# Kernel tuning notes

Hardware: AMD Instinct MI355X
Metric: run time of the kernel (lower is better)

The kernel has to match this reference:

```python
import jax, jax.numpy as jnp
import numpy as np

N_NODES = 81920
N_EDGES = 1310720
NODES_PER_GRAPH = 320
N_GRAPHS = N_NODES // NODES_PER_GRAPH  # 256
IN_DIM = 64
HID = 64
OUT = 64


def setup_inputs() -> dict:
    key = jax.random.key(0)
    ks = jax.random.split(key, 16)
    x = jax.random.normal(ks[0], (N_NODES, IN_DIM), dtype=jnp.float32)
    edge_index = jax.random.randint(ks[1], (2, N_EDGES), 0, N_NODES, dtype=jnp.int32)
    # sorted graph-membership vector: 256 graphs of 320 nodes each
    batch = (jnp.arange(N_NODES, dtype=jnp.int32) // NODES_PER_GRAPH)
    std = 1.0  # module re-inits nn.Linear weights with N(0, 1)
    dims = [(IN_DIM, HID), (HID, HID), (HID, OUT)]
    params = {}
    for i, (di, do) in enumerate(dims):
        params[f"Wl{i}"] = std * jax.random.normal(ks[2 + 3 * i], (di, do), dtype=jnp.float32)
        params[f"bl{i}"] = jnp.zeros((do,), dtype=jnp.float32)
        params[f"Wr{i}"] = std * jax.random.normal(ks[3 + 3 * i], (di, do), dtype=jnp.float32)
    return dict(x=x, edge_index=edge_index, batch=batch, **params)


def _sage_conv(x, src, dst, Wl, bl, Wr):
    # PyG SAGEConv (aggr='mean', root_weight=True):
    #   out = lin_l(mean_{j in N(i)} x_j) + lin_r(x_i)
    msg = x[src]                                              # [E, d] gather
    agg = jax.ops.segment_sum(msg, dst, num_segments=N_NODES)  # [N, d] scatter-add
    cnt = jax.ops.segment_sum(jnp.ones((src.shape[0],), x.dtype), dst,
                              num_segments=N_NODES)
    agg = agg / jnp.maximum(cnt, 1.0)[:, None]                # mean aggregation
    return agg @ Wl + bl + x @ Wr


def reference(x, edge_index, batch, Wl0, bl0, Wr0, Wl1, bl1, Wr1, Wl2, bl2, Wr2):
    src, dst = edge_index[0], edge_index[1]
    layers = [(Wl0, bl0, Wr0), (Wl1, bl1, Wr1), (Wl2, bl2, Wr2)]
    h = x
    for i, (Wl, bl, Wr) in enumerate(layers):
        h = _sage_conv(h, src, dst, Wl, bl, Wr)
        if i < len(layers) - 1:
            h = jax.nn.relu(h)
            # F.dropout is identity in eval mode (training=False)
    # unbatch + take node 0 of every graph: first index where batch == g
    first_idx = jnp.searchsorted(batch, jnp.arange(N_GRAPHS, dtype=batch.dtype))
    return h[first_idx]  # [N_GRAPHS, OUT]
```

## Files before the change

kernel.cpp:

```cpp
#include <hip/hip_runtime.h>

#define N_NODES 81920
#define N_EDGES 1310720
#define NG 256
#define D 64
#define TM 64
#define SA 65
#define SB 33
#define NB 320
#define NBLK 1280
#define BMW 2560
#define HCHUNK 4096
#define EPT 16
#define CAP0 1280
#define CAP1 256
#define CAP2 64

typedef __attribute__((ext_vector_type(2))) short sbf2;

__device__ __forceinline__ bool tb(const unsigned* bm, int i) {
    return (bm[i >> 5] >> (i & 31)) & 1u;
}
__device__ __forceinline__ unsigned bf16rne(float f) {
    unsigned u = __float_as_uint(f);
    return (u + 0x7fffu + ((u >> 16) & 1u)) >> 16;
}


__global__ __launch_bounds__(256) void init_ws(float4* __restrict__ aggb4,
                                               unsigned* __restrict__ bms,
                                               int* __restrict__ indeg,
                                               int* __restrict__ n01,
                                               int* __restrict__ cur0,
                                               int* __restrict__ cur1,
                                               int* __restrict__ cur2,
                                               const float2* __restrict__ x2,
                                               unsigned* __restrict__ xb) {
    int t = blockIdx.x * 256 + threadIdx.x;
    float4 z = make_float4(0.f, 0.f, 0.f, 0.f);
    aggb4[t] = z;
    aggb4[t + NBLK * 256] = z;
    if (t < 3 * BMW) bms[t] = 0u;
    if (t < N_NODES) indeg[t] = 0;
    if (t < 2) n01[t] = 0;
    if (t < NBLK) {
        cur0[t] = t * CAP0;
        cur1[t] = t * CAP1;
        cur2[t] = t * CAP2;
    }
    #pragma unroll
    for (int i = 0; i < 8; ++i) {
        int idx = i * (NBLK * 256) + t;
        float2 v = x2[idx];
        xb[idx] = bf16rne(v.x) | (bf16rne(v.y) << 16);
    }
}


__global__ void ff_mark(const int* __restrict__ batch, int* __restrict__ fidx,
                        unsigned* __restrict__ bm2, unsigned* __restrict__ bm1,
                        float* __restrict__ aggf) {
    int i = blockIdx.x * 256 + threadIdx.x;
    int b = batch[i];
    if (i == 0 || batch[i - 1] != b) {
        fidx[b] = i;
        unsigned bit = 1u << (i & 31);
        atomicOr(&bm2[i >> 5], bit);
        atomicOr(&bm1[i >> 5], bit);
        float4* r = (float4*)&aggf[i * D];
        #pragma unroll
        for (int j = 0; j < 16; ++j) r[j] = make_float4(0.f, 0.f, 0.f, 0.f);
    }
}

__global__ void mark_srcs_bm(const int* __restrict__ src, const int* __restrict__ dst,
                             const unsigned* __restrict__ bmD, unsigned* __restrict__ bmS,
                             const unsigned* __restrict__ orsrc) {
    if (orsrc && blockIdx.x == 0) {
        for (int w = threadIdx.x; w < BMW; w += 256)
            if (orsrc[w]) atomicOr(&bmS[w], orsrc[w]);
    }
    int e = blockIdx.x * 256 + threadIdx.x;
    if (e < N_EDGES && tb(bmD, dst[e])) {
        int s = src[e];
        atomicOr(&bmS[s >> 5], 1u << (s & 31));
    }
}


__global__ __launch_bounds__(256) void build(const int* __restrict__ src,
                                             const int* __restrict__ dst,
                                             const unsigned* __restrict__ bm0,
                                             const unsigned* __restrict__ bm1,
                                             const unsigned* __restrict__ bm2,
                                             int* __restrict__ cur0,
                                             int* __restrict__ cur1,
                                             int* __restrict__ cur2,
                                             int* __restrict__ esp0,
                                             int* __restrict__ esp1,
                                             int* __restrict__ esp2,
                                             int* __restrict__ indeg,
                                             int* __restrict__ list1,
                                             int* __restrict__ n1) {
    __shared__ int h0[NBLK];
    __shared__ int b0[NBLK];
    const int tid = threadIdx.x;
    const int e0  = blockIdx.x * HCHUNK;

    for (int i = tid; i < NBLK; i += 256) h0[i] = 0;

    {
        int i = blockIdx.x * 256 + tid;
        int lane = tid & 63;
        bool p1 = tb(bm1, i);
        unsigned long long b1 = __ballot(p1);
        int lt = __popcll(b1 & ((1ull << lane) - 1));
        int base = 0;
        if (lane == 0 && b1) base = atomicAdd(n1, __popcll(b1));
        base = __shfl(base, 0);
        if (p1) list1[base + lt] = i;
    }
    __syncthreads();

    int pk_r[EPT];
    int sb_r[EPT];
    int rk_r[EPT];

    #pragma unroll
    for (int j = 0; j < EPT; ++j) {
        int e = e0 + j * 256 + tid;
        int d = dst[e];
        sb_r[j] = -1;
        if (tb(bm0, d)) {
            int s  = src[e];
            int sb = s >> 6;
            int pk = (d << 6) | (s & 63);
            pk_r[j] = pk;
            sb_r[j] = sb;
            rk_r[j] = atomicAdd(&h0[sb], 1);
            atomicAdd(&indeg[d], 1);
            if (tb(bm1, d)) {
                int p1 = atomicAdd(&cur1[sb], 1);
                if (p1 < sb * CAP1 + CAP1) esp1[p1] = pk;
                if (tb(bm2, d)) {
                    int p2 = atomicAdd(&cur2[sb], 1);
                    if (p2 < sb * CAP2 + CAP2) esp2[p2] = pk;
                }
            }
        }
    }
    __syncthreads();

    for (int i = tid; i < NBLK; i += 256) {
        int c = h0[i];
        b0[i] = c ? atomicAdd(&cur0[i], c) : 0;
    }
    __syncthreads();

    #pragma unroll
    for (int j = 0; j < EPT; ++j) {
        int sb = sb_r[j];
        if (sb >= 0) {
            int pos = b0[sb] + rk_r[j];
            if (pos < sb * CAP0 + CAP0) esp0[pos] = pk_r[j];
        }
    }
}


__global__ __launch_bounds__(256, 8) void sage_push_bf_pre(
    const unsigned* __restrict__ xb, const int* __restrict__ cur,
    const int* __restrict__ esp, unsigned* __restrict__ aggb, int cap)
{
    __shared__ unsigned Rs[TM * SB];

    const int tid  = threadIdx.x;
    const int base = blockIdx.x * TM;
    const int lane = tid & 63;
    const int w    = tid >> 6;
    const int l5   = lane & 31;
    const int hi   = lane >> 5;

    const int e0 = blockIdx.x * cap;
    const int e1 = min(cur[blockIdx.x], e0 + cap);
    if (e0 == e1) return;

    for (int idx = tid; idx < TM * 32; idx += 256) {
        int m = idx >> 5, k = idx & 31;
        Rs[m * SB + k] = xb[(base << 5) + idx];
    }
    __syncthreads();

    const int chunk = ((e1 - e0) + 3) >> 2;
    int e = e0 + w * chunk;
    const int ee = min(e + chunk, e1);

    for (; e + 64 <= ee; e += 64) {
        int pv = esp[e + lane];
        #pragma unroll
        for (int u = 0; u < 32; ++u) {
            int p = __shfl(pv, (u << 1) + hi);
            unsigned v = Rs[(p & 63) * SB + l5];
            __builtin_amdgcn_global_atomic_fadd_v2bf16(
                (sbf2*)&aggb[((p >> 6) << 5) + l5], *(sbf2*)&v);
        }
    }
    for (; e < ee; ++e) {
        int p = esp[e];
        if (!hi) {
            unsigned v = Rs[(p & 63) * SB + l5];
            __builtin_amdgcn_global_atomic_fadd_v2bf16(
                (sbf2*)&aggb[((p >> 6) << 5) + l5], *(sbf2*)&v);
        }
    }
}


__global__ __launch_bounds__(256, 8) void sage_push_bf(
    const float* __restrict__ hin, const int* __restrict__ cur,
    const int* __restrict__ esp, unsigned* __restrict__ aggb, int cap)
{
    __shared__ unsigned Rs[TM * SB];

    const int tid  = threadIdx.x;
    const int base = blockIdx.x * TM;
    const int lane = tid & 63;
    const int w    = tid >> 6;
    const int l5   = lane & 31;
    const int hi   = lane >> 5;

    const int e0 = blockIdx.x * cap;
    const int e1 = min(cur[blockIdx.x], e0 + cap);
    if (e0 == e1) return;

    for (int idx = tid; idx < TM * 32; idx += 256) {
        int m = idx >> 5, k = idx & 31;
        float2 v = *(const float2*)&hin[((base + m) << 6) + (k << 1)];
        Rs[m * SB + k] = bf16rne(v.x) | (bf16rne(v.y) << 16);
    }
    __syncthreads();

    const int chunk = ((e1 - e0) + 3) >> 2;
    int e = e0 + w * chunk;
    const int ee = min(e + chunk, e1);

    for (; e + 64 <= ee; e += 64) {
        int pv = esp[e + lane];
        #pragma unroll
        for (int u = 0; u < 32; ++u) {
            int p = __shfl(pv, (u << 1) + hi);
            unsigned v = Rs[(p & 63) * SB + l5];
            __builtin_amdgcn_global_atomic_fadd_v2bf16(
                (sbf2*)&aggb[((p >> 6) << 5) + l5], *(sbf2*)&v);
        }
    }
    for (; e < ee; ++e) {
        int p = esp[e];
        if (!hi) {
            unsigned v = Rs[(p & 63) * SB + l5];
            __builtin_amdgcn_global_atomic_fadd_v2bf16(
                (sbf2*)&aggb[((p >> 6) << 5) + l5], *(sbf2*)&v);
        }
    }
}


__global__ __launch_bounds__(256, 8) void sage_push_f32(
    const float* __restrict__ hin, const int* __restrict__ cur,
    const int* __restrict__ esp, float* __restrict__ agg, int cap)
{
    __shared__ float Rs[TM * SA];

    const int tid  = threadIdx.x;
    const int base = blockIdx.x * TM;
    const int lane = tid & 63;
    const int w    = tid >> 6;

    const int e0 = blockIdx.x * cap;
    const int e1 = min(cur[blockIdx.x], e0 + cap);
    if (e0 == e1) return;

    for (int idx = tid; idx < TM * D; idx += 256) {
        int m = idx >> 6, k = idx & 63;
        Rs[m * SA + k] = hin[(base << 6) + idx];
    }
    __syncthreads();

    const int chunk = ((e1 - e0) + 3) >> 2;
    int e = e0 + w * chunk;
    const int ee = min(e + chunk, e1);

    for (; e < ee; ++e) {
        int p = esp[e];
        atomicAdd(&agg[(p & 0x7fffffc0) + lane], Rs[(p & 63) * SA + lane]);
    }
}


__global__ __launch_bounds__(256, 4) void sage_finish_dense(
    const unsigned* __restrict__ xb, unsigned* __restrict__ aggb,
    const int* __restrict__ indeg, float* __restrict__ hout,
    const float* __restrict__ Wl, const float* __restrict__ bl,
    const float* __restrict__ Wr)
{
    __shared__ float As[TM * SA];
    __shared__ float Xs[TM * SA];
    __shared__ float invs[TM];

    const int tid  = threadIdx.x;
    const int base = blockIdx.x * TM;

    if (tid < TM) invs[tid] = 1.0f / (float)max(indeg[base + tid], 1);
    for (int idx = tid; idx < TM * 32; idx += 256) {
        int m = idx >> 5, k2 = (idx & 31) << 1;
        unsigned v = aggb[(base << 5) + idx];
        As[m * SA + k2]     = __uint_as_float(v << 16);
        As[m * SA + k2 + 1] = __uint_as_float(v & 0xffff0000u);
        aggb[(base << 5) + idx] = 0u;
        unsigned xw = xb[(base << 5) + idx];
        Xs[m * SA + k2]     = __uint_as_float(xw << 16);
        Xs[m * SA + k2 + 1] = __uint_as_float(xw & 0xffff0000u);
    }
    __syncthreads();
    for (int idx = tid; idx < TM * D; idx += 256) {
        int m = idx >> 6, k = idx & 63;
        As[m * SA + k] *= invs[m];
    }
    __syncthreads();

    const int j0 = (tid & 15) << 2;
    const int m0 = (tid >> 4) << 2;
    float o[4][4];
    float4 b4 = *(const float4*)&bl[j0];
    #pragma unroll
    for (int mi = 0; mi < 4; ++mi) {
        o[mi][0] = b4.x; o[mi][1] = b4.y; o[mi][2] = b4.z; o[mi][3] = b4.w;
    }
    #pragma unroll 8
    for (int k = 0; k < D; ++k) {
        float4 wl = *(const float4*)&Wl[(k << 6) + j0];
        float4 wr = *(const float4*)&Wr[(k << 6) + j0];
        #pragma unroll
        for (int mi = 0; mi < 4; ++mi) {
            float a = As[(m0 + mi) * SA + k];
            float x = Xs[(m0 + mi) * SA + k];
            o[mi][0] += a * wl.x + x * wr.x;
            o[mi][1] += a * wl.y + x * wr.y;
            o[mi][2] += a * wl.z + x * wr.z;
            o[mi][3] += a * wl.w + x * wr.w;
        }
    }
    #pragma unroll
    for (int mi = 0; mi < 4; ++mi) {
        float4 r = make_float4(fmaxf(o[mi][0], 0.f), fmaxf(o[mi][1], 0.f),
                               fmaxf(o[mi][2], 0.f), fmaxf(o[mi][3], 0.f));
        *(float4*)&hout[(base + m0 + mi) * D + j0] = r;
    }
}


__global__ __launch_bounds__(256, 4) void sage_finish_sel(
    const float* __restrict__ hin, unsigned* __restrict__ aggb,
    const int* __restrict__ indeg, const int* __restrict__ list,
    const int* __restrict__ pcount, float* __restrict__ hout,
    const float* __restrict__ Wl, const float* __restrict__ bl,
    const float* __restrict__ Wr)
{
    __shared__ float As[TM * SA];
    __shared__ float Xs[TM * SA];
    __shared__ float invs[TM];
    __shared__ int   nid[TM];

    const int cntv = *pcount;
    const int base = blockIdx.x * TM;
    if (base >= cntv) return;

    const int tid = threadIdx.x;
    if (tid < TM) {
        int n = (base + tid < cntv) ? list[base + tid] : -1;
        nid[tid]  = n;
        invs[tid] = (n >= 0) ? 1.0f / (float)max(indeg[n], 1) : 0.f;
    }
    __syncthreads();
    for (int idx = tid; idx < TM * 32; idx += 256) {
        int m = idx >> 5, k2 = idx & 31;
        int n = nid[m];
        if (n >= 0) {
            unsigned v = aggb[(n << 5) + k2];
            As[m * SA + (k2 << 1)]     = __uint_as_float(v << 16) * invs[m];
            As[m * SA + (k2 << 1) + 1] = __uint_as_float(v & 0xffff0000u) * invs[m];
        } else {
            As[m * SA + (k2 << 1)]     = 0.f;
            As[m * SA + (k2 << 1) + 1] = 0.f;
        }
    }
    for (int idx = tid; idx < TM * D; idx += 256) {
        int m = idx >> 6, k = idx & 63;
        int n = nid[m];
        Xs[m * SA + k] = (n >= 0) ? hin[n * D + k] : 0.f;
    }
    __syncthreads();

    const int j0 = (tid & 15) << 2;
    const int m0 = (tid >> 4) << 2;
    float o[4][4];
    float4 b4 = *(const float4*)&bl[j0];
    #pragma unroll
    for (int mi = 0; mi < 4; ++mi) {
        o[mi][0] = b4.x; o[mi][1] = b4.y; o[mi][2] = b4.z; o[mi][3] = b4.w;
    }
    #pragma unroll 8
    for (int k = 0; k < D; ++k) {
        float4 wl = *(const float4*)&Wl[(k << 6) + j0];
        float4 wr = *(const float4*)&Wr[(k << 6) + j0];
        #pragma unroll
        for (int mi = 0; mi < 4; ++mi) {
            float a = As[(m0 + mi) * SA + k];
            float x = Xs[(m0 + mi) * SA + k];
            o[mi][0] += a * wl.x + x * wr.x;
            o[mi][1] += a * wl.y + x * wr.y;
            o[mi][2] += a * wl.z + x * wr.z;
            o[mi][3] += a * wl.w + x * wr.w;
        }
    }
    #pragma unroll
    for (int mi = 0; mi < 4; ++mi) {
        int n = nid[m0 + mi];
        if (n >= 0) {
            float4 r = make_float4(fmaxf(o[mi][0], 0.f), fmaxf(o[mi][1], 0.f),
                                   fmaxf(o[mi][2], 0.f), fmaxf(o[mi][3], 0.f));
            *(float4*)&hout[n * D + j0] = r;
        }
    }
}


__global__ __launch_bounds__(256, 3) void final_gemm_sel(
    const float* __restrict__ hin, const float* __restrict__ agg,
    const int* __restrict__ indeg, const int* __restrict__ fidx,
    const float* __restrict__ Wl, const float* __restrict__ bl,
    const float* __restrict__ Wr, float* __restrict__ out)
{
    __shared__ float As[TM * SA];
    __shared__ float Xs[TM * SA];
    __shared__ int   nid[TM];
    __shared__ float invs[TM];

    const int tid  = threadIdx.x;
    const int base = blockIdx.x * TM;

    if (tid < TM) {
        int n = fidx[base + tid];
        nid[tid]  = n;
        invs[tid] = 1.0f / (float)max(indeg[n], 1);
    }
    __syncthreads();
    for (int idx = tid; idx < TM * D; idx += 256) {
        int m = idx >> 6, k = idx & 63;
        int n = nid[m];
        As[m * SA + k] = agg[n * D + k] * invs[m];
        Xs[m * SA + k] = hin[n * D + k];
    }
    __syncthreads();

    const int j0 = (tid & 15) << 2;
    const int m0 = (tid >> 4) << 2;
    float o[4][4];
    float4 b4 = *(const float4*)&bl[j0];
    #pragma unroll
    for (int mi = 0; mi < 4; ++mi) {
        o[mi][0] = b4.x; o[mi][1] = b4.y; o[mi][2] = b4.z; o[mi][3] = b4.w;
    }
    #pragma unroll 8
    for (int k = 0; k < D; ++k) {
        float4 wl = *(const float4*)&Wl[(k << 6) + j0];
        float4 wr = *(const float4*)&Wr[(k << 6) + j0];
        #pragma unroll
        for (int mi = 0; mi < 4; ++mi) {
            float a = As[(m0 + mi) * SA + k];
            float x = Xs[(m0 + mi) * SA + k];
            o[mi][0] += a * wl.x + x * wr.x;
            o[mi][1] += a * wl.y + x * wr.y;
            o[mi][2] += a * wl.z + x * wr.z;
            o[mi][3] += a * wl.w + x * wr.w;
        }
    }
    #pragma unroll
    for (int mi = 0; mi < 4; ++mi) {
        float4 r = make_float4(o[mi][0], o[mi][1], o[mi][2], o[mi][3]);
        *(float4*)&out[(base + m0 + mi) * D + j0] = r;
    }
}


extern "C" void kernel_launch(void* const* d_in, const int* in_sizes, int n_in,
                              void* d_out, int out_size, void* d_ws, size_t ws_size,
                              hipStream_t stream)
{
    const float* x     = (const float*)d_in[0];
    const int*   ei    = (const int*)d_in[1];
    const int*   batch = (const int*)d_in[2];
    const float* Wl0 = (const float*)d_in[3];
    const float* bl0 = (const float*)d_in[4];
    const float* Wr0 = (const float*)d_in[5];
    const float* Wl1 = (const float*)d_in[6];
    const float* bl1 = (const float*)d_in[7];
    const float* Wr1 = (const float*)d_in[8];
    const float* Wl2 = (const float*)d_in[9];
    const float* bl2 = (const float*)d_in[10];
    const float* Wr2 = (const float*)d_in[11];
    float* out = (float*)d_out;

    const int* src = ei;
    const int* dst = ei + N_EDGES;

    char* ws = (char*)d_ws;
    size_t off = 0;
    auto alloc = [&](size_t bytes) -> void* {
        void* p = ws + off;
        off = (off + bytes + 255) & ~(size_t)255;
        return p;
    };
    int*      cur0  = (int*)alloc(NBLK * sizeof(int));
    int*      cur1  = (int*)alloc(NBLK * sizeof(int));
    int*      cur2  = (int*)alloc(NBLK * sizeof(int));
    int*      fidx  = (int*)alloc(NG * sizeof(int));
    int*      list1 = (int*)alloc(N_NODES * sizeof(int));
    int*      esp0  = (int*)alloc((size_t)NBLK * CAP0 * sizeof(int));
    int*      esp1  = (int*)alloc((size_t)NBLK * CAP1 * sizeof(int));
    int*      esp2  = (int*)alloc((size_t)NBLK * CAP2 * sizeof(int));
    unsigned* aggb  = (unsigned*)alloc((size_t)N_NODES * 32 * sizeof(unsigned));
    float*    aggf  = (float*)alloc((size_t)N_NODES * D * sizeof(float));
    float*    h1    = (float*)alloc((size_t)N_NODES * D * sizeof(float));
    float*    h2    = (float*)alloc((size_t)N_NODES * D * sizeof(float));
    unsigned* bms   = (unsigned*)alloc((size_t)3 * BMW * sizeof(unsigned));
    int*      indeg = (int*)alloc(N_NODES * sizeof(int));
    int*      n01   = (int*)alloc(64 * sizeof(int));
    unsigned* bm0 = bms;
    unsigned* bm1 = bms + BMW;
    unsigned* bm2 = bms + 2 * BMW;
    int* n1 = n01 + 1;
    unsigned* xb = (unsigned*)h2;
    (void)ws_size; (void)in_sizes; (void)n_in; (void)out_size;

    const int EB = (N_EDGES + 255) / 256;

    init_ws<<<NBLK, 256, 0, stream>>>((float4*)aggb, bms, indeg, n01,
                                      cur0, cur1, cur2, (const float2*)x, xb);
    ff_mark<<<NB, 256, 0, stream>>>(batch, fidx, bm2, bm1, aggf);
    mark_srcs_bm<<<EB, 256, 0, stream>>>(src, dst, bm2, bm1, (const unsigned*)nullptr);
    mark_srcs_bm<<<EB, 256, 0, stream>>>(src, dst, bm1, bm0, bm1);
    build<<<NB, 256, 0, stream>>>(src, dst, bm0, bm1, bm2, cur0, cur1, cur2,
                                  esp0, esp1, esp2, indeg, list1, n1);

    sage_push_bf_pre <<<NBLK, 256, 0, stream>>>(xb, cur0, esp0, aggb, CAP0);
    sage_finish_dense<<<NBLK, 256, 0, stream>>>(xb, aggb, indeg, h1, Wl0, bl0, Wr0);
    sage_push_bf     <<<NBLK, 256, 0, stream>>>(h1, cur1, esp1, aggb, CAP1);
    sage_finish_sel  <<<NBLK, 256, 0, stream>>>(h1, aggb, indeg, list1, n1,
                                                h2, Wl1, bl1, Wr1);
    sage_push_f32    <<<NBLK, 256, 0, stream>>>(h2, cur2, esp2, aggf, CAP2);
    final_gemm_sel   <<<NG / TM, 256, 0, stream>>>(h2, aggf, indeg, fidx, Wl2, bl2, Wr2, out);
}
```

Before: 411.8 us.

## Replace layer-0 global atomic push with staged gather and dst-side LDS reduction

Layer 0 now buckets each relevant edge twice, by destination block and by source block. A stage kernel copies each source's bf16 row, read from LDS, into a per-edge staging buffer. A reduce kernel then accumulates those rows per destination block in LDS with shared-memory atomics, computes in-degree itself, and fuses the mean, the GEMM and the ReLU. This removes the global bf16 atomic scatter to aggb and its separate finish pass, at the cost of a large staging buffer (about 200MB), an extra edge list, and extra global write and read traffic. The new path runs only if the workspace is large enough; otherwise the old push path is used.

```diff
diff --git a/kernel.cpp b/kernel.cpp
--- a/kernel.cpp
+++ b/kernel.cpp
@@ -7,6 +7,7 @@
 #define TM 64
 #define SA 65
 #define SB 33
+#define SC 36
 #define NB 320
 #define NBLK 1280
 #define BMW 2560
@@ -25,6 +26,8 @@
     unsigned u = __float_as_uint(f);
     return (u + 0x7fffu + ((u >> 16) & 1u)) >> 16;
 }
+__device__ __forceinline__ float bfl(unsigned u) { return __uint_as_float(u << 16); }
+__device__ __forceinline__ float bfh(unsigned u) { return __uint_as_float(u & 0xffff0000u); }
 
 
 __global__ __launch_bounds__(256) void init_ws(float4* __restrict__ aggb4,
@@ -32,6 +35,7 @@
                                                int* __restrict__ indeg,
                                                int* __restrict__ n01,
                                                int* __restrict__ cur0,
+                                               int* __restrict__ curS,
                                                int* __restrict__ cur1,
                                                int* __restrict__ cur2,
                                                const float2* __restrict__ x2,
@@ -45,6 +49,7 @@
     if (t < 2) n01[t] = 0;
     if (t < NBLK) {
         cur0[t] = t * CAP0;
+        curS[t] = t * CAP0;
         cur1[t] = t * CAP1;
         cur2[t] = t * CAP2;
     }
@@ -88,20 +93,106 @@
 }
 
 
-__global__ __launch_bounds__(256) void build(const int* __restrict__ src,
-                                             const int* __restrict__ dst,
-                                             const unsigned* __restrict__ bm0,
-                                             const unsigned* __restrict__ bm1,
-                                             const unsigned* __restrict__ bm2,
-                                             int* __restrict__ cur0,
-                                             int* __restrict__ cur1,
-                                             int* __restrict__ cur2,
-                                             int* __restrict__ esp0,
-                                             int* __restrict__ esp1,
-                                             int* __restrict__ esp2,
-                                             int* __restrict__ indeg,
-                                             int* __restrict__ list1,
-                                             int* __restrict__ n1) {
+__global__ __launch_bounds__(256) void build_staged(
+    const int* __restrict__ src, const int* __restrict__ dst,
+    const unsigned* __restrict__ bm0, const unsigned* __restrict__ bm1,
+    const unsigned* __restrict__ bm2,
+    int* __restrict__ cur0, int* __restrict__ curS,
+    int* __restrict__ cur1, int* __restrict__ cur2,
+    int* __restrict__ esp0, int* __restrict__ espS,
+    int* __restrict__ esp1, int* __restrict__ esp2,
+    int* __restrict__ list1, int* __restrict__ n1)
+{
+    __shared__ int hd[NBLK];
+    __shared__ int hs[NBLK];
+    __shared__ int bd[NBLK];
+    __shared__ int bs[NBLK];
+    const int tid = threadIdx.x;
+    const int e0  = blockIdx.x * HCHUNK;
+
+    for (int i = tid; i < NBLK; i += 256) { hd[i] = 0; hs[i] = 0; }
+
+    {
+        int i = blockIdx.x * 256 + tid;
+        int lane = tid & 63;
+        bool p1 = tb(bm1, i);
+        unsigned long long b1 = __ballot(p1);
+        int lt = __popcll(b1 & ((1ull << lane) - 1));
+        int base = 0;
+        if (lane == 0 && b1) base = atomicAdd(n1, __popcll(b1));
+        base = __shfl(base, 0);
+        if (p1) list1[base + lt] = i;
+    }
+    __syncthreads();
+
+    int pk_r[EPT];
+    int md_r[EPT];
+    int ms_r[EPT];
+
+    #pragma unroll
+    for (int j = 0; j < EPT; ++j) {
+        int e = e0 + j * 256 + tid;
+        int d = dst[e];
+        md_r[j] = -1;
+        if (tb(bm0, d)) {
+            int s  = src[e];
+            int db = d >> 6;
+            int sb = s >> 6;
+            pk_r[j] = (s << 6) | (d & 63);
+            md_r[j] = db | (atomicAdd(&hd[db], 1) << 11);
+            ms_r[j] = sb | (atomicAdd(&hs[sb], 1) << 11);
+            if (tb(bm1, d)) {
+                int pk = (d << 6) | (s & 63);
+                int p1 = atomicAdd(&cur1[sb], 1);
+                if (p1 < sb * CAP1 + CAP1) esp1[p1] = pk;
+                if (tb(bm2, d)) {
+                    int p2 = atomicAdd(&cur2[sb], 1);
+                    if (p2 < sb * CAP2 + CAP2) esp2[p2] = pk;
+                }
+            }
+        }
+    }
+    __syncthreads();
+
+    for (int i = tid; i < NBLK; i += 256) {
+        int cd = hd[i];
+        bd[i] = cd ? atomicAdd(&cur0[i], cd) : 0;
+        int cs = hs[i];
+        bs[i] = cs ? atomicAdd(&curS[i], cs) : 0;
+    }
+    __syncthreads();
+
+    #pragma unroll
+    for (int j = 0; j < EPT; ++j) {
+        int md = md_r[j];
+        if (md >= 0) {
+            int db = md & 2047;
+            int sb = ms_r[j] & 2047;
+            int posd = bd[db] + (md >> 11);
+            int poss = bs[sb] + (ms_r[j] >> 11);
+            if (posd < db * CAP0 + CAP0 && poss < sb * CAP0 + CAP0) {
+                esp0[posd] = pk_r[j];
+                espS[poss] = (posd << 6) | ((pk_r[j] >> 6) & 63);
+            }
+        }
+    }
+}
+
+
+__global__ __launch_bounds__(256) void build_push(const int* __restrict__ src,
+                                                  const int* __restrict__ dst,
+                                                  const unsigned* __restrict__ bm0,
+                                                  const unsigned* __restrict__ bm1,
+                                                  const unsigned* __restrict__ bm2,
+                                                  int* __restrict__ cur0,
+                                                  int* __restrict__ cur1,
+                                                  int* __restrict__ cur2,
+                                                  int* __restrict__ esp0,
+                                                  int* __restrict__ esp1,
+                                                  int* __restrict__ esp2,
+                                                  int* __restrict__ indeg,
+                                                  int* __restrict__ list1,
+                                                  int* __restrict__ n1) {
     __shared__ int h0[NBLK];
     __shared__ int b0[NBLK];
     const int tid = threadIdx.x;
@@ -168,6 +259,177 @@
 }
 
 
+__global__ __launch_bounds__(256, 8) void sage_stage_l0(
+    const unsigned* __restrict__ xb, const int* __restrict__ curS,
+    const int* __restrict__ espS, uint4* __restrict__ stage)
+{
+    __shared__ unsigned Rs[TM * SC];
+
+    const int tid  = threadIdx.x;
+    const int base = blockIdx.x * TM;
+    const int lane = tid & 63;
+    const int w    = tid >> 6;
+    const int g    = lane >> 3;
+    const int l3   = lane & 7;
+
+    const int e0 = blockIdx.x * CAP0;
+    const int e1 = min(curS[blockIdx.x], e0 + CAP0);
+    if (e0 == e1) return;
+
+    for (int idx = tid; idx < TM * 32; idx += 256) {
+        int m = idx >> 5, k = idx & 31;
+        Rs[m * SC + k] = xb[(base << 5) + idx];
+    }
+    __syncthreads();
+
+    const int chunk = ((e1 - e0) + 3) >> 2;
+    int e = e0 + w * chunk;
+    const int ee = min(e + chunk, e1);
+
+    for (; e + 64 <= ee; e += 64) {
+        int pv = espS[e + lane];
+        #pragma unroll
+        for (int u = 0; u < 8; ++u) {
+            int p = __shfl(pv, (u << 3) + g);
+            uint4 v = *(const uint4*)&Rs[(p & 63) * SC + (l3 << 2)];
+            stage[((p >> 6) << 3) + l3] = v;
+        }
+    }
+    for (; e < ee; ++e) {
+        int p = espS[e];
+        if (lane < 8) {
+            uint4 v = *(const uint4*)&Rs[(p & 63) * SC + (lane << 2)];
+            stage[((p >> 6) << 3) + lane] = v;
+        }
+    }
+}
+
+
+__global__ __launch_bounds__(256, 4) void sage_reduce_l0(
+    const unsigned* __restrict__ xb, const int* __restrict__ cur0,
+    const int* __restrict__ esp0, const uint4* __restrict__ stage,
+    int* __restrict__ indeg, float* __restrict__ hout,
+    const float* __restrict__ Wl, const float* __restrict__ bl,
+    const float* __restrict__ Wr)
+{
+    __shared__ float As[TM * SA];
+    __shared__ float Xs[TM * SA];
+    __shared__ float invs[TM];
+
+    const int tid  = threadIdx.x;
+    const int base = blockIdx.x * TM;
+    const int lane = tid & 63;
+    const int w    = tid >> 6;
+    const int g    = lane >> 3;
+    const int l3   = lane & 7;
+
+    for (int idx = tid; idx < TM * SA; idx += 256) As[idx] = 0.f;
+    for (int idx = tid; idx < TM * 32; idx += 256) {
+        int m = idx >> 5, k2 = (idx & 31) << 1;
+        unsigned xw = xb[(base << 5) + idx];
+        Xs[m * SA + k2]     = bfl(xw);
+        Xs[m * SA + k2 + 1] = bfh(xw);
+    }
+    __syncthreads();
+
+    const int e0 = blockIdx.x * CAP0;
+    const int e1 = min(cur0[blockIdx.x], e0 + CAP0);
+
+    const int chunk = ((e1 - e0) + 3) >> 2;
+    int e = e0 + w * chunk;
+    const int ee = min(e + chunk, e1);
+
+    for (; e + 64 <= ee; e += 64) {
+        int pv = esp0[e + lane];
+        #pragma unroll
+        for (int u = 0; u < 8; ++u) {
+            int ei = (u << 3) + g;
+            int p  = __shfl(pv, ei);
+            uint4 v = stage[((e + ei) << 3) + l3];
+            int dl = p & 63;
+            float* row = &As[dl * SA + (l3 << 3)];
+            atomicAdd(&row[0], bfl(v.x));
+            atomicAdd(&row[1], bfh(v.x));
+            atomicAdd(&row[2], bfl(v.y));
+            atomicAdd(&row[3], bfh(v.y));
+            atomicAdd(&row[4], bfl(v.z));
+            atomicAdd(&row[5], bfh(v.z));
+            atomicAdd(&row[6], bfl(v.w));
+            atomicAdd(&row[7], bfh(v.w));
+            if (l3 == 0) atomicAdd(&As[dl * SA + 64], 1.0f);
+        }
+    }
+    for (; e < ee; ++e) {
+        int p = esp0[e];
+        if (lane < 8) {
+            uint4 v = stage[(e << 3) + lane];
+            int dl = p & 63;
+            float* row = &As[dl * SA + (lane << 3)];
+            atomicAdd(&row[0], bfl(v.x));
+            atomicAdd(&row[1], bfh(v.x));
+            atomicAdd(&row[2], bfl(v.y));
+            atomicAdd(&row[3], bfh(v.y));
+            atomicAdd(&row[4], bfl(v.z));
+            atomicAdd(&row[5], bfh(v.z));
+            atomicAdd(&row[6], bfl(v.w));
+            atomicAdd(&row[7], bfh(v.w));
+            if (lane == 0) atomicAdd(&As[dl * SA + 64], 1.0f);
+        }
+    }
+    __syncthreads();
+
+    if (tid < TM) {
+        int cn = (int)As[tid * SA + 64];
+        indeg[base + tid] = cn;
+        invs[tid] = 1.0f / (float)max(cn, 1);
+    }
+    __syncthreads();
+
+    const int j0 = (tid & 7) << 3;
+    const int m2 = (tid >> 3) << 1;
+    const float iv0 = invs[m2];
+    const float iv1 = invs[m2 + 1];
+    float o[2][8];
+    {
+        float4 ba = *(const float4*)&bl[j0];
+        float4 bb = *(const float4*)&bl[j0 + 4];
+        #pragma unroll
+        for (int mi = 0; mi < 2; ++mi) {
+            o[mi][0] = ba.x; o[mi][1] = ba.y; o[mi][2] = ba.z; o[mi][3] = ba.w;
+            o[mi][4] = bb.x; o[mi][5] = bb.y; o[mi][6] = bb.z; o[mi][7] = bb.w;
+        }
+    }
+    #pragma unroll 8
+    for (int k = 0; k < D; ++k) {
+        float a0 = As[m2 * SA + k] * iv0;
+        float a1 = As[(m2 + 1) * SA + k] * iv1;
+        float x0 = Xs[m2 * SA + k];
+        float x1 = Xs[(m2 + 1) * SA + k];
+        float4 wl0 = *(const float4*)&Wl[(k << 6) + j0];
+        float4 wl1 = *(const float4*)&Wl[(k << 6) + j0 + 4];
+        float4 wr0 = *(const float4*)&Wr[(k << 6) + j0];
+        float4 wr1 = *(const float4*)&Wr[(k << 6) + j0 + 4];
+        o[0][0] += a0 * wl0.x + x0 * wr0.x;  o[1][0] += a1 * wl0.x + x1 * wr0.x;
+        o[0][1] += a0 * wl0.y + x0 * wr0.y;  o[1][1] += a1 * wl0.y + x1 * wr0.y;
+        o[0][2] += a0 * wl0.z + x0 * wr0.z;  o[1][2] += a1 * wl0.z + x1 * wr0.z;
+        o[0][3] += a0 * wl0.w + x0 * wr0.w;  o[1][3] += a1 * wl0.w + x1 * wr0.w;
+        o[0][4] += a0 * wl1.x + x0 * wr1.x;  o[1][4] += a1 * wl1.x + x1 * wr1.x;
+        o[0][5] += a0 * wl1.y + x0 * wr1.y;  o[1][5] += a1 * wl1.y + x1 * wr1.y;
+        o[0][6] += a0 * wl1.z + x0 * wr1.z;  o[1][6] += a1 * wl1.z + x1 * wr1.z;
+        o[0][7] += a0 * wl1.w + x0 * wr1.w;  o[1][7] += a1 * wl1.w + x1 * wr1.w;
+    }
+    #pragma unroll
+    for (int mi = 0; mi < 2; ++mi) {
+        float4 r0 = make_float4(fmaxf(o[mi][0], 0.f), fmaxf(o[mi][1], 0.f),
+                                fmaxf(o[mi][2], 0.f), fmaxf(o[mi][3], 0.f));
+        float4 r1 = make_float4(fmaxf(o[mi][4], 0.f), fmaxf(o[mi][5], 0.f),
+                                fmaxf(o[mi][6], 0.f), fmaxf(o[mi][7], 0.f));
+        *(float4*)&hout[(base + m2 + mi) * D + j0]     = r0;
+        *(float4*)&hout[(base + m2 + mi) * D + j0 + 4] = r1;
+    }
+}
+
+
 __global__ __launch_bounds__(256, 8) void sage_push_bf_pre(
     const unsigned* __restrict__ xb, const int* __restrict__ cur,
     const int* __restrict__ esp, unsigned* __restrict__ aggb, int cap)
@@ -314,12 +576,12 @@
     for (int idx = tid; idx < TM * 32; idx += 256) {
         int m = idx >> 5, k2 = (idx & 31) << 1;
         unsigned v = aggb[(base << 5) + idx];
-        As[m * SA + k2]     = __uint_as_float(v << 16);
-        As[m * SA + k2 + 1] = __uint_as_float(v & 0xffff0000u);
+        As[m * SA + k2]     = bfl(v);
+        As[m * SA + k2 + 1] = bfh(v);
         aggb[(base << 5) + idx] = 0u;
         unsigned xw = xb[(base << 5) + idx];
-        Xs[m * SA + k2]     = __uint_as_float(xw << 16);
-        Xs[m * SA + k2 + 1] = __uint_as_float(xw & 0xffff0000u);
+        Xs[m * SA + k2]     = bfl(xw);
+        Xs[m * SA + k2 + 1] = bfh(xw);
     }
     __syncthreads();
     for (int idx = tid; idx < TM * D; idx += 256) {
@@ -387,8 +649,8 @@
         int n = nid[m];
         if (n >= 0) {
             unsigned v = aggb[(n << 5) + k2];
-            As[m * SA + (k2 << 1)]     = __uint_as_float(v << 16) * invs[m];
-            As[m * SA + (k2 << 1) + 1] = __uint_as_float(v & 0xffff0000u) * invs[m];
+            As[m * SA + (k2 << 1)]     = bfl(v) * invs[m];
+            As[m * SA + (k2 << 1) + 1] = bfh(v) * invs[m];
         } else {
             As[m * SA + (k2 << 1)]     = 0.f;
             As[m * SA + (k2 << 1) + 1] = 0.f;
@@ -522,11 +784,13 @@
         return p;
     };
     int*      cur0  = (int*)alloc(NBLK * sizeof(int));
+    int*      curS  = (int*)alloc(NBLK * sizeof(int));
     int*      cur1  = (int*)alloc(NBLK * sizeof(int));
     int*      cur2  = (int*)alloc(NBLK * sizeof(int));
     int*      fidx  = (int*)alloc(NG * sizeof(int));
     int*      list1 = (int*)alloc(N_NODES * sizeof(int));
     int*      esp0  = (int*)alloc((size_t)NBLK * CAP0 * sizeof(int));
+    int*      espS  = (int*)alloc((size_t)NBLK * CAP0 * sizeof(int));
     int*      esp1  = (int*)alloc((size_t)NBLK * CAP1 * sizeof(int));
     int*      esp2  = (int*)alloc((size_t)NBLK * CAP2 * sizeof(int));
     unsigned* aggb  = (unsigned*)alloc((size_t)N_NODES * 32 * sizeof(unsigned));
@@ -536,25 +800,37 @@
     unsigned* bms   = (unsigned*)alloc((size_t)3 * BMW * sizeof(unsigned));
     int*      indeg = (int*)alloc(N_NODES * sizeof(int));
     int*      n01   = (int*)alloc(64 * sizeof(int));
+    uint4*    stage = (uint4*)alloc((size_t)NBLK * CAP0 * 128);
+    const bool staged = (off <= ws_size);
     unsigned* bm0 = bms;
     unsigned* bm1 = bms + BMW;
     unsigned* bm2 = bms + 2 * BMW;
     int* n1 = n01 + 1;
     unsigned* xb = (unsigned*)h2;
-    (void)ws_size; (void)in_sizes; (void)n_in; (void)out_size;
+    (void)in_sizes; (void)n_in; (void)out_size;
 
     const int EB = (N_EDGES + 255) / 256;
 
     init_ws<<<NBLK, 256, 0, stream>>>((float4*)aggb, bms, indeg, n01,
-                                      cur0, cur1, cur2, (const float2*)x, xb);
+                                      cur0, curS, cur1, cur2, (const float2*)x, xb);
     ff_mark<<<NB, 256, 0, stream>>>(batch, fidx, bm2, bm1, aggf);
     mark_srcs_bm<<<EB, 256, 0, stream>>>(src, dst, bm2, bm1, (const unsigned*)nullptr);
     mark_srcs_bm<<<EB, 256, 0, stream>>>(src, dst, bm1, bm0, bm1);
-    build<<<NB, 256, 0, stream>>>(src, dst, bm0, bm1, bm2, cur0, cur1, cur2,
-                                  esp0, esp1, esp2, indeg, list1, n1);
-
-    sage_push_bf_pre <<<NBLK, 256, 0, stream>>>(xb, cur0, esp0, aggb, CAP0);
-    sage_finish_dense<<<NBLK, 256, 0, stream>>>(xb, aggb, indeg, h1, Wl0, bl0, Wr0);
+
+    if (staged) {
+        build_staged<<<NB, 256, 0, stream>>>(src, dst, bm0, bm1, bm2,
+                                             cur0, curS, cur1, cur2,
+                                             esp0, espS, esp1, esp2, list1, n1);
+        sage_stage_l0 <<<NBLK, 256, 0, stream>>>(xb, curS, espS, stage);
+        sage_reduce_l0<<<NBLK, 256, 0, stream>>>(xb, cur0, esp0, stage,
+                                                 indeg, h1, Wl0, bl0, Wr0);
+    } else {
+        build_push<<<NB, 256, 0, stream>>>(src, dst, bm0, bm1, bm2, cur0, cur1, cur2,
+                                           esp0, esp1, esp2, indeg, list1, n1);
+        sage_push_bf_pre <<<NBLK, 256, 0, stream>>>(xb, cur0, esp0, aggb, CAP0);
+        sage_finish_dense<<<NBLK, 256, 0, stream>>>(xb, aggb, indeg, h1, Wl0, bl0, Wr0);
+    }
+
     sage_push_bf     <<<NBLK, 256, 0, stream>>>(h1, cur1, esp1, aggb, CAP1);
     sage_finish_sel  <<<NBLK, 256, 0, stream>>>(h1, aggb, indeg, list1, n1,
                                                 h2, Wl1, bl1, Wr1);
```

Result: no change. 416.8 us (+1.2%).
